# Kernel optimization log

Measured on AMD Instinct MI355X. Metric: run time of the kernel, lower is better.

## Reference

```python
import jax, jax.numpy as jnp
import numpy as np

D_MODEL = 1024
NUM_HEADS = 16
HEAD_DIM = D_MODEL // NUM_HEADS
SCALE = HEAD_DIM ** -0.5
LN_EPS = 1e-5
Q_EPS = 1e-5


def bit_quant(W):
    # BitNet b1.58 ternary weight quantization with straight-through estimator.
    gamma = jnp.mean(jnp.abs(W))
    Wq = jnp.clip(jnp.round(W / (gamma + Q_EPS)), -1.0, 1.0) * gamma
    return W + jax.lax.stop_gradient(Wq - W)


def layer_norm(x, gamma, beta):
    mu = jnp.mean(x, axis=-1, keepdims=True)
    var = jnp.mean(jnp.square(x - mu), axis=-1, keepdims=True)
    return (x - mu) * jax.lax.rsqrt(var + LN_EPS) * gamma + beta


def setup_inputs() -> dict:
    key = jax.random.key(0)
    ks = jax.random.split(key, 8)
    B, T, T_ctx, C = 4, 1024, 2048, D_MODEL
    w_std = C ** -0.5
    return {
        "x": jax.random.normal(ks[0], (B, T, C), jnp.float32),
        "context": jax.random.normal(ks[1], (B, T_ctx, C), jnp.float32),
        "Wq": jax.random.normal(ks[2], (C, C), jnp.float32) * w_std,
        "bq": jnp.zeros((C,), jnp.float32),
        "Wk": jax.random.normal(ks[3], (C, C), jnp.float32) * w_std,
        "bk": jnp.zeros((C,), jnp.float32),
        "Wv": jax.random.normal(ks[4], (C, C), jnp.float32) * w_std,
        "bv": jnp.zeros((C,), jnp.float32),
        "Wo": jax.random.normal(ks[5], (C, C), jnp.float32) * w_std,
        "bo": jnp.zeros((C,), jnp.float32),
        "ln_gamma": jnp.ones((C,), jnp.float32),
        "ln_beta": jnp.zeros((C,), jnp.float32),
    }


def reference(x, context, Wq, bq, Wk, bk, Wv, bv, Wo, bo, ln_gamma, ln_beta):
    B, T, C = x.shape
    T_ctx = context.shape[1]
    residual = x
    xn = layer_norm(x, ln_gamma, ln_beta)
    # BitNet-quantized projections (torch Linear: y = x @ W.T + b)
    q = xn @ bit_quant(Wq).T + bq                      # [B,T,C]
    k = context @ bit_quant(Wk).T + bk                 # [B,T_ctx,C]
    v = context @ bit_quant(Wv).T + bv                 # [B,T_ctx,C]
    q = q.reshape(B, T, NUM_HEADS, HEAD_DIM)
    k = k.reshape(B, T_ctx, NUM_HEADS, HEAD_DIM)
    v = v.reshape(B, T_ctx, NUM_HEADS, HEAD_DIM)
    scores = jnp.einsum("bqhd,bkhd->bhqk", q, k) * SCALE   # [B,H,T,T_ctx]
    probs = jax.nn.softmax(scores, axis=-1)
    out = jnp.einsum("bhqk,bkhd->bqhd", probs, v).reshape(B, T, C)
    return residual + (out @ bit_quant(Wo).T + bo)
```

## Files before the change

### kernel.cpp

```cpp
#include <hip/hip_runtime.h>
#include <hip/hip_bf16.h>

typedef __attribute__((ext_vector_type(8))) short s8x;
typedef __attribute__((ext_vector_type(4))) float f4x;
typedef unsigned short u16;
typedef unsigned int u32;

#define T_ 1024
#define TC_ 2048
#define SCLOG2E 0.1803368801111243f

#define WAIT_VM(n) asm volatile("s_waitcnt vmcnt(" #n ")" ::: "memory")

__device__ __forceinline__ u16 f2bf(float f) {
    u32 u = __float_as_uint(f);
    return (u16)((u + 0x7fffu + ((u >> 16) & 1u)) >> 16);
}

#if defined(__has_builtin)
#if __has_builtin(__builtin_amdgcn_cvt_pk_bf16_f32)
#define HAVE_PK 1
#endif
#endif

__device__ __forceinline__ u32 pack2bf(float a, float b) {
#ifdef HAVE_PK
    typedef __attribute__((ext_vector_type(2))) __bf16 bf2t;
    bf2t r = __builtin_amdgcn_cvt_pk_bf16_f32(a, b);
    u32 u;
    __builtin_memcpy(&u, &r, 4);
    return u;
#else
    return (u32)f2bf(a) | ((u32)f2bf(b) << 16);
#endif
}

__device__ __forceinline__ void gload16(const void* g, void* l) {
    __builtin_amdgcn_global_load_lds((const __attribute__((address_space(1))) u32*)g,
                                     (__attribute__((address_space(3))) u32*)l, 16, 0, 0);
}

__global__ __launch_bounds__(256) void absmean_k(const float* __restrict__ W0, const float* __restrict__ W1,
                                                 const float* __restrict__ W2, const float* __restrict__ W3,
                                                 float* __restrict__ gsum) {
    int wi = blockIdx.y;
    const float* W = (wi == 0) ? W0 : (wi == 1) ? W1 : (wi == 2) ? W2 : W3;
    const int n4 = (1024 * 1024) / 4;
    float s = 0.f;
    int stride = gridDim.x * blockDim.x;
    for (int i = blockIdx.x * blockDim.x + threadIdx.x; i < n4; i += stride) {
        float4 v = ((const float4*)W)[i];
        s += fabsf(v.x) + fabsf(v.y) + fabsf(v.z) + fabsf(v.w);
    }
#pragma unroll
    for (int off = 32; off; off >>= 1) s += __shfl_down(s, off, 64);
    __shared__ float ps[4];
    if ((threadIdx.x & 63) == 0) ps[threadIdx.x >> 6] = s;
    __syncthreads();
    if (threadIdx.x == 0) atomicAdd(gsum + wi, ps[0] + ps[1] + ps[2] + ps[3]);
}

__global__ __launch_bounds__(256) void prep_k(
        const float* __restrict__ x, const float* __restrict__ lng, const float* __restrict__ lnb,
        u16* __restrict__ xn,
        const float* __restrict__ ctx, u16* __restrict__ ctxb,
        const float* __restrict__ W0, const float* __restrict__ W1,
        const float* __restrict__ W2, const float* __restrict__ W3,
        u16* __restrict__ D0, u16* __restrict__ D1, u16* __restrict__ D2, u16* __restrict__ D3,
        const float* __restrict__ gsum) {
    __shared__ float ps[8];
    int bx = blockIdx.x, t = threadIdx.x;
    if (bx < 4096) {
        int row = bx;
        float4 xv = ((const float4*)(x + (long)row * 1024))[t];
        float s = xv.x + xv.y + xv.z + xv.w;
        float s2 = xv.x * xv.x + xv.y * xv.y + xv.z * xv.z + xv.w * xv.w;
#pragma unroll
        for (int off = 32; off; off >>= 1) { s += __shfl_down(s, off, 64); s2 += __shfl_down(s2, off, 64); }
        if ((t & 63) == 0) { ps[t >> 6] = s; ps[4 + (t >> 6)] = s2; }
        __syncthreads();
        float S = ps[0] + ps[1] + ps[2] + ps[3];
        float S2 = ps[4] + ps[5] + ps[6] + ps[7];
        float mu = S * (1.f / 1024.f);
        float var = S2 * (1.f / 1024.f) - mu * mu;
        float rstd = rsqrtf(var + 1e-5f);
        float4 gv = ((const float4*)lng)[t];
        float4 bv = ((const float4*)lnb)[t];
        uint2 o;
        o.x = pack2bf((xv.x - mu) * rstd * gv.x + bv.x, (xv.y - mu) * rstd * gv.y + bv.y);
        o.y = pack2bf((xv.z - mu) * rstd * gv.z + bv.z, (xv.w - mu) * rstd * gv.w + bv.w);
        ((uint2*)(xn + (long)row * 1024))[t] = o;
    } else if (bx < 12288) {
        int i = (bx - 4096) * 256 + t;
        float4 v = ((const float4*)ctx)[i];
        uint2 o = {pack2bf(v.x, v.y), pack2bf(v.z, v.w)};
        ((uint2*)ctxb)[i] = o;
    } else {
        int wi = (bx - 12288) >> 10;
        const float* W = (wi == 0) ? W0 : (wi == 1) ? W1 : (wi == 2) ? W2 : W3;
        u16* D = (wi == 0) ? D0 : (wi == 1) ? D1 : (wi == 2) ? D2 : D3;
        float inv = 1.0f / (gsum[wi] * (1.0f / 1048576.0f) + 1e-5f);
        int i = ((bx - 12288) & 1023) * 256 + t;
        float4 wv = ((const float4*)W)[i];
        uint2 o;
        o.x = pack2bf(fminf(1.f, fmaxf(-1.f, rintf(wv.x * inv))),
                      fminf(1.f, fmaxf(-1.f, rintf(wv.y * inv))));
        o.y = pack2bf(fminf(1.f, fmaxf(-1.f, rintf(wv.z * inv))),
                      fminf(1.f, fmaxf(-1.f, rintf(wv.w * inv))));
        ((uint2*)D)[i] = o;
    }
}

__global__ __launch_bounds__(256) void gemm_fused(
        const u16* __restrict__ xn, const u16* __restrict__ ctxb,
        const u16* __restrict__ wtq, const u16* __restrict__ wtk, const u16* __restrict__ wtv,
        const float* __restrict__ bq, const float* __restrict__ bk, const float* __restrict__ bv,
        const float* __restrict__ gsum,
        u16* __restrict__ qb, u16* __restrict__ kb, u16* __restrict__ vtb) {
    __shared__ __align__(16) char smem[49152];
    int tid = threadIdx.x;
    int w = tid >> 6, l = tid & 63, lq = l & 15, lh = l >> 4;
    int wm = (w >> 1) * 64, wn = (w & 1) * 64;
    int bx = blockIdx.x;
    int xcd = bx & 7;
    int prob, m0, n0, gidx;
    const u16 *A, *Wt;
    const float* bias;
    float sc;
    if (bx < 256) {
        int local = bx >> 3;
        prob = 0; A = xn; Wt = wtq; bias = bq; sc = SCLOG2E; gidx = 0;
        m0 = (xcd * 4 + (local & 3)) * 128;
        n0 = (local >> 2) * 128;
    } else {
        int b = bx - 256;
        int local3 = b >> 3;
        int kv = local3 & 1;
        int idx = local3 >> 1;
        prob = 1 + kv; A = ctxb;
        Wt = kv ? wtv : wtk; bias = kv ? bv : bk; sc = 1.0f; gidx = 1 + kv;
        m0 = (xcd * 8 + (idx & 7)) * 128;
        n0 = (idx >> 3) * 128;
    }
    int sp = tid >> 3, ss = tid & 7;
    int st = ss ^ (sp & 7);
    int r0 = sp * 2 + (st >> 2), c0 = st & 3;
    const u16* Ag0 = A + (long)(m0 + r0) * 1024 + c0 * 8;
    const u16* Ag1 = Ag0 + 64 * 1024;
    const u16* Bg0 = Wt + (long)(n0 + r0) * 1024 + c0 * 8;
    const u16* Bg1 = Bg0 + 64 * 1024;
    int aoff[4], boff[4];
#pragma unroll
    for (int i = 0; i < 4; i++) {
        int ar = wm + i * 16 + lq, ap = ar >> 1;
        aoff[i] = ap * 128 + (((((ar & 1) << 2) | lh) ^ (ap & 7)) * 16);
        int br = wn + i * 16 + lq, bp = br >> 1;
        boff[i] = bp * 128 + (((((br & 1) << 2) | lh) ^ (bp & 7)) * 16);
    }
    f4x acc[4][4] = {};
#define STAGE_G(kt, buf)                                                   \
    {                                                                      \
        char* Ad = smem + (buf) * 16384;                                   \
        char* Bd = Ad + 8192;                                              \
        gload16(Ag0 + (kt) * 32, Ad + tid * 16);                           \
        gload16(Ag1 + (kt) * 32, Ad + 4096 + tid * 16);                    \
        gload16(Bg0 + (kt) * 32, Bd + tid * 16);                           \
        gload16(Bg1 + (kt) * 32, Bd + 4096 + tid * 16);                    \
    }
    STAGE_G(0, 0);
    STAGE_G(1, 1);
#pragma unroll
    for (int kt = 0; kt < 32; kt++) {
        if (kt < 31) { WAIT_VM(4); } else { WAIT_VM(0); }
        __builtin_amdgcn_s_barrier();
        if (kt + 2 < 32) STAGE_G(kt + 2, (kt + 2) % 3);
        const char* Ac = smem + (kt % 3) * 16384;
        const char* Bc = Ac + 8192;
        s8x af[4], bfr[4];
#pragma unroll
        for (int i = 0; i < 4; i++) {
            af[i] = *(const s8x*)(Ac + aoff[i]);
            bfr[i] = *(const s8x*)(Bc + boff[i]);
        }
#pragma unroll
        for (int i = 0; i < 4; i++)
#pragma unroll
            for (int j = 0; j < 4; j++)
                acc[i][j] = __builtin_amdgcn_mfma_f32_16x16x32_bf16(af[i], bfr[j], acc[i][j], 0, 0, 0);
    }
    float gamma = gsum[gidx] * (1.0f / 1048576.0f) * sc;
    if (prob < 2) {
        u16* outq = (prob == 0) ? qb : kb;
        int tshift = (prob == 0) ? 10 : 11;
        int tmask = (1 << tshift) - 1;
#pragma unroll
        for (int i = 0; i < 4; i++) {
            int gr = m0 + wm + i * 16 + lh * 4;
#pragma unroll
            for (int j = 0; j < 4; j++) {
                int gc = n0 + wn + j * 16 + lq;
                float bb = bias[gc] * sc;
                int h = gc >> 6, d = gc & 63;
#pragma unroll
                for (int r = 0; r < 4; r++) {
                    int row = gr + r;
                    int bidx = row >> tshift, tt = row & tmask;
                    outq[((((long)(bidx * 16 + h)) << tshift) + tt) * 64 + d] = f2bf(acc[i][j][r] * gamma + bb);
                }
            }
        }
    } else {
        __syncthreads();
        char* Ct = smem;
#pragma unroll
        for (int i = 0; i < 4; i++) {
            int tt = wm + i * 16 + lh * 4;
#pragma unroll
            for (int j = 0; j < 4; j++) {
                int c = wn + j * 16 + lq;
                float bb = bias[n0 + c];
                uint2 pk;
                pk.x = pack2bf(acc[i][j][0] * gamma + bb, acc[i][j][1] * gamma + bb);
                pk.y = pack2bf(acc[i][j][2] * gamma + bb, acc[i][j][3] * gamma + bb);
                int slot = (tt >> 3) ^ (c & 15);
                *(uint2*)(Ct + c * 256 + slot * 16 + (tt & 7) * 2) = pk;
            }
        }
        __syncthreads();
        int bb2 = m0 >> 11, t0 = m0 & 2047;
#pragma unroll
        for (int it = 0; it < 8; it++) {
            int e = it * 256 + tid;
            int c = e >> 4, ch = e & 15;
            int slot = ch ^ (c & 15);
            s8x v = *(const s8x*)(Ct + c * 256 + slot * 16);
            int gcg = n0 + c;
            int h = gcg >> 6, d = gcg & 63;
            *(s8x*)(vtb + ((long)((bb2 * 16 + h) * 64 + d)) * TC_ + t0 + ch * 8) = v;
        }
    }
}

__global__ __launch_bounds__(256) void gemm_o(const u16* __restrict__ A, const u16* __restrict__ Wt,
                                              const float* __restrict__ bias, const float* __restrict__ gsum,
                                              const float* __restrict__ residual, float* __restrict__ outr) {
    __shared__ __align__(16) char smem[36864];
    int tid = threadIdx.x;
    int w = tid >> 6, l = tid & 63, lq = l & 15, lh = l >> 4;
    int wm = (w >> 1) * 64, wn = (w & 1) * 32;
    int bx = blockIdx.x;
    int xcd = bx & 7, local = bx >> 3;
    int m0 = (xcd * 4 + (local & 3)) * 128;
    int n0 = (local >> 2) * 64;
    int sp = tid >> 3, ss = tid & 7;
    int st = ss ^ (sp & 7);
    int r0 = sp * 2 + (st >> 2), c0 = st & 3;
    const u16* Ag0 = A + (long)(m0 + r0) * 1024 + c0 * 8;
    const u16* Ag1 = Ag0 + 64 * 1024;
    const u16* Bg0 = Wt + (long)(n0 + r0) * 1024 + c0 * 8;
    int aoff[4], boff[2];
#pragma unroll
    for (int i = 0; i < 4; i++) {
        int ar = wm + i * 16 + lq, ap = ar >> 1;
        aoff[i] = ap * 128 + (((((ar & 1) << 2) | lh) ^ (ap & 7)) * 16);
    }
#pragma unroll
    for (int j = 0; j < 2; j++) {
        int br = wn + j * 16 + lq, bp = br >> 1;
        boff[j] = bp * 128 + (((((br & 1) << 2) | lh) ^ (bp & 7)) * 16);
    }
    f4x acc[4][2] = {};
#define STAGE_O(kt, buf)                                                   \
    {                                                                      \
        char* Ad = smem + (buf) * 12288;                                   \
        char* Bd = Ad + 8192;                                              \
        gload16(Ag0 + (kt) * 32, Ad + tid * 16);                           \
        gload16(Ag1 + (kt) * 32, Ad + 4096 + tid * 16);                    \
        gload16(Bg0 + (kt) * 32, Bd + tid * 16);                           \
    }
    STAGE_O(0, 0);
    STAGE_O(1, 1);
#pragma unroll
    for (int kt = 0; kt < 32; kt++) {
        if (kt < 31) { WAIT_VM(3); } else { WAIT_VM(0); }
        __builtin_amdgcn_s_barrier();
        if (kt + 2 < 32) STAGE_O(kt + 2, (kt + 2) % 3);
        const char* Ac = smem + (kt % 3) * 12288;
        const char* Bc = Ac + 8192;
        s8x af[4], bfr[2];
#pragma unroll
        for (int i = 0; i < 4; i++) af[i] = *(const s8x*)(Ac + aoff[i]);
#pragma unroll
        for (int j = 0; j < 2; j++) bfr[j] = *(const s8x*)(Bc + boff[j]);
#pragma unroll
        for (int i = 0; i < 4; i++)
#pragma unroll
            for (int j = 0; j < 2; j++)
                acc[i][j] = __builtin_amdgcn_mfma_f32_16x16x32_bf16(af[i], bfr[j], acc[i][j], 0, 0, 0);
    }
    float gamma = gsum[3] * (1.0f / 1048576.0f);
#pragma unroll
    for (int i = 0; i < 4; i++) {
        int gr = m0 + wm + i * 16 + lh * 4;
#pragma unroll
        for (int j = 0; j < 2; j++) {
            int gc = n0 + wn + j * 16 + lq;
            float bb = bias[gc];
#pragma unroll
            for (int r = 0; r < 4; r++) {
                long idx = (long)(gr + r) * 1024 + gc;
                outr[idx] = residual[idx] + acc[i][j][r] * gamma + bb;
            }
        }
    }
}

__global__ __launch_bounds__(256) void attn_k(const u16* __restrict__ qh, const u16* __restrict__ kh,
                                              const u16* __restrict__ vth, u16* __restrict__ attn) {
    __shared__ __align__(16) char smem[51200];
    int tid = threadIdx.x, w = tid >> 6, l = tid & 63, lq = l & 15, lh = l >> 4;
    int bh = blockIdx.x, q0 = blockIdx.y * 128;
    const u16* qp = qh + ((long)bh * T_ + q0) * 64;
    const u16* kp = kh + (long)bh * TC_ * 64;
    const u16* vp = vth + (long)bh * 64 * TC_;
#pragma unroll
    for (int i = 0; i < 4; i++) {
        int cid = i * 256 + tid;
        int r = cid >> 3, c = (cid & 7) ^ (r & 7);
        gload16(qp + r * 64 + c * 8, smem + cid * 16);
    }
    __syncthreads();
    s8x qf[2][2];
#pragma unroll
    for (int nb = 0; nb < 2; nb++)
#pragma unroll
        for (int dh = 0; dh < 2; dh++) {
            int qrow = w * 32 + nb * 16 + lq;
            int ch = (dh * 4 + lh) ^ (qrow & 7);
            qf[nb][dh] = *(const s8x*)(smem + qrow * 128 + ch * 16);
        }
    __syncthreads();
#define STAGE_KV(kt, buf)                                                          \
    {                                                                              \
        char* Kb = smem + (buf) * 16384;                                           \
        char* Vb = Kb + 8192;                                                      \
        _Pragma("unroll") for (int i = 0; i < 2; i++) {                            \
            int cid = i * 256 + tid;                                               \
            int r = cid >> 3, c = (cid & 7) ^ (r & 7);                             \
            gload16(kp + ((kt) * 64 + r) * 64 + c * 8, Kb + cid * 16);             \
            gload16(vp + (long)r * TC_ + (kt) * 64 + c * 8, Vb + cid * 16);        \
        }                                                                          \
    }
    STAGE_KV(0, 0);
    f4x oacc[2][4] = {};
    f4x lrun[2] = {};
    const s8x ones = {16256, 16256, 16256, 16256, 16256, 16256, 16256, 16256};
    char* Psb = smem + 32768 + w * 4608;
    for (int kt = 0; kt < TC_ / 64; kt++) {
        __syncthreads();
        if (kt + 1 < TC_ / 64) STAGE_KV(kt + 1, (kt + 1) & 1);
        char* Ksb = smem + (kt & 1) * 16384;
        char* Vsb = Ksb + 8192;
        f4x z[2][4];
#pragma unroll
        for (int ni = 0; ni < 4; ni++) {
            int kr = ni * 16 + lq;
            s8x a0 = *(const s8x*)(Ksb + kr * 128 + ((lh) ^ (kr & 7)) * 16);
            s8x a1 = *(const s8x*)(Ksb + kr * 128 + ((4 + lh) ^ (kr & 7)) * 16);
#pragma unroll
            for (int nb = 0; nb < 2; nb++) {
                f4x zz = {0.f, 0.f, 0.f, 0.f};
                zz = __builtin_amdgcn_mfma_f32_16x16x32_bf16(a0, qf[nb][0], zz, 0, 0, 0);
                zz = __builtin_amdgcn_mfma_f32_16x16x32_bf16(a1, qf[nb][1], zz, 0, 0, 0);
                z[nb][ni] = zz;
            }
        }
#pragma unroll
        for (int nb = 0; nb < 2; nb++) {
            int prow = nb * 16 + lq;
#pragma unroll
            for (int ni = 0; ni < 4; ni++) {
                uint2 pk;
                pk.x = pack2bf(__builtin_amdgcn_exp2f(z[nb][ni][0]), __builtin_amdgcn_exp2f(z[nb][ni][1]));
                pk.y = pack2bf(__builtin_amdgcn_exp2f(z[nb][ni][2]), __builtin_amdgcn_exp2f(z[nb][ni][3]));
                *(uint2*)(Psb + prow * 144 + ni * 32 + lh * 8) = pk;
            }
        }
        s8x vf[4][2];
#pragma unroll
        for (int nd = 0; nd < 4; nd++) {
            int vr = nd * 16 + lq;
            vf[nd][0] = *(const s8x*)(Vsb + vr * 128 + ((lh) ^ (vr & 7)) * 16);
            vf[nd][1] = *(const s8x*)(Vsb + vr * 128 + ((4 + lh) ^ (vr & 7)) * 16);
        }
#pragma unroll
        for (int qb = 0; qb < 2; qb++) {
            int prow = qb * 16 + lq;
            s8x pf0 = *(const s8x*)(Psb + prow * 144 + lh * 16);
            s8x pf1 = *(const s8x*)(Psb + prow * 144 + 64 + lh * 16);
            f4x rs = {0.f, 0.f, 0.f, 0.f};
            rs = __builtin_amdgcn_mfma_f32_16x16x32_bf16(pf0, ones, rs, 0, 0, 0);
            rs = __builtin_amdgcn_mfma_f32_16x16x32_bf16(pf1, ones, rs, 0, 0, 0);
#pragma unroll
            for (int r = 0; r < 4; r++) lrun[qb][r] += rs[r];
#pragma unroll
            for (int nd = 0; nd < 4; nd++) {
                oacc[qb][nd] = __builtin_amdgcn_mfma_f32_16x16x32_bf16(pf0, vf[nd][0], oacc[qb][nd], 0, 0, 0);
                oacc[qb][nd] = __builtin_amdgcn_mfma_f32_16x16x32_bf16(pf1, vf[nd][1], oacc[qb][nd], 0, 0, 0);
            }
        }
    }
    int b = bh >> 4, h = bh & 15;
#pragma unroll
    for (int qb = 0; qb < 2; qb++)
#pragma unroll
        for (int r = 0; r < 4; r++) {
            int q = q0 + w * 32 + qb * 16 + lh * 4 + r;
            float rcp = 1.f / lrun[qb][r];
#pragma unroll
            for (int nd = 0; nd < 4; nd++)
                attn[((long)(b * T_ + q)) * 1024 + h * 64 + nd * 16 + lq] = f2bf(oacc[qb][nd][r] * rcp);
        }
}

extern "C" void kernel_launch(void* const* d_in, const int* in_sizes, int n_in,
                              void* d_out, int out_size, void* d_ws, size_t ws_size,
                              hipStream_t stream) {
    const float* x   = (const float*)d_in[0];
    const float* ctx = (const float*)d_in[1];
    const float* Wq  = (const float*)d_in[2];
    const float* bq  = (const float*)d_in[3];
    const float* Wk  = (const float*)d_in[4];
    const float* bk  = (const float*)d_in[5];
    const float* Wv  = (const float*)d_in[6];
    const float* bv  = (const float*)d_in[7];
    const float* Wo  = (const float*)d_in[8];
    const float* bo  = (const float*)d_in[9];
    const float* lng = (const float*)d_in[10];
    const float* lnb = (const float*)d_in[11];
    float* out = (float*)d_out;

    char* ws = (char*)d_ws;
    float* gsum = (float*)ws;
    size_t off = 256;
    u16* wtq  = (u16*)(ws + off); off += (size_t)1024 * 1024 * 2;
    u16* wtk  = (u16*)(ws + off); off += (size_t)1024 * 1024 * 2;
    u16* wtv  = (u16*)(ws + off); off += (size_t)1024 * 1024 * 2;
    u16* wto  = (u16*)(ws + off); off += (size_t)1024 * 1024 * 2;
    u16* ctxb = (u16*)(ws + off); off += (size_t)8192 * 1024 * 2;
    u16* xn   = (u16*)(ws + off); off += (size_t)4096 * 1024 * 2;
    u16* qb_  = (u16*)(ws + off); off += (size_t)4096 * 1024 * 2;
    u16* kb   = (u16*)(ws + off); off += (size_t)8192 * 1024 * 2;
    u16* vtb  = (u16*)(ws + off); off += (size_t)8192 * 1024 * 2;
    u16* attnb = xn;

    hipMemsetAsync(gsum, 0, 16, stream);
    absmean_k<<<dim3(128, 4), 256, 0, stream>>>(Wq, Wk, Wv, Wo, gsum);
    prep_k<<<16384, 256, 0, stream>>>(x, lng, lnb, xn, ctx, ctxb,
                                      Wq, Wk, Wv, Wo, wtq, wtk, wtv, wto, gsum);
    gemm_fused<<<1280, 256, 0, stream>>>(xn, ctxb, wtq, wtk, wtv, bq, bk, bv, gsum, qb_, kb, vtb);
    attn_k<<<dim3(64, 8), 256, 0, stream>>>(qb_, kb, vtb, attnb);
    gemm_o<<<512, 256, 0, stream>>>(attnb, wto, bo, gsum, x, out);
}
```

Before: 254.2 us.

## Keep attention probabilities in registers via permlane swaps, halve query tile

The attention kernel no longer writes exp'd scores to LDS and reads them back as MFMA A-operands. It rearranges them in registers with permlane32/permlane16 swaps, and adds s_setprio around the MFMA sections. The query tile per block drops from 128 to 64 rows (16 per wave), doubling the grid, shrinking LDS to 32KB and raising occupancy. The cost is that each K/V tile is now loaded by twice as many blocks, so K/V global and LDS traffic is doubled per unit of compute.

```diff
diff --git a/kernel.cpp b/kernel.cpp
--- a/kernel.cpp
+++ b/kernel.cpp
@@ -20,6 +20,9 @@
 #if defined(__has_builtin)
 #if __has_builtin(__builtin_amdgcn_cvt_pk_bf16_f32)
 #define HAVE_PK 1
+#endif
+#if __has_builtin(__builtin_amdgcn_permlane16_swap) && __has_builtin(__builtin_amdgcn_permlane32_swap)
+#define HAVE_PLSWAP 1
 #endif
 #endif
 
@@ -32,6 +35,25 @@
     return u;
 #else
     return (u32)f2bf(a) | ((u32)f2bf(b) << 16);
+#endif
+}
+
+__device__ __forceinline__ void pswap32(u32& a, u32& b) {
+#ifdef HAVE_PLSWAP
+    typedef __attribute__((ext_vector_type(2))) unsigned int u2x;
+    u2x r = __builtin_amdgcn_permlane32_swap(a, b, false, false);
+    a = r.x; b = r.y;
+#else
+    asm("v_permlane32_swap_b32 %0, %1" : "+v"(a), "+v"(b));
+#endif
+}
+__device__ __forceinline__ void pswap16(u32& a, u32& b) {
+#ifdef HAVE_PLSWAP
+    typedef __attribute__((ext_vector_type(2))) unsigned int u2x;
+    u2x r = __builtin_amdgcn_permlane16_swap(a, b, false, false);
+    a = r.x; b = r.y;
+#else
+    asm("v_permlane16_swap_b32 %0, %1" : "+v"(a), "+v"(b));
 #endif
 }
 
@@ -317,28 +339,26 @@
 
 __global__ __launch_bounds__(256) void attn_k(const u16* __restrict__ qh, const u16* __restrict__ kh,
                                               const u16* __restrict__ vth, u16* __restrict__ attn) {
-    __shared__ __align__(16) char smem[51200];
+    __shared__ __align__(16) char smem[32768];
     int tid = threadIdx.x, w = tid >> 6, l = tid & 63, lq = l & 15, lh = l >> 4;
-    int bh = blockIdx.x, q0 = blockIdx.y * 128;
+    int bh = blockIdx.x, q0 = blockIdx.y * 64;
     const u16* qp = qh + ((long)bh * T_ + q0) * 64;
     const u16* kp = kh + (long)bh * TC_ * 64;
     const u16* vp = vth + (long)bh * 64 * TC_;
 #pragma unroll
-    for (int i = 0; i < 4; i++) {
+    for (int i = 0; i < 2; i++) {
         int cid = i * 256 + tid;
         int r = cid >> 3, c = (cid & 7) ^ (r & 7);
         gload16(qp + r * 64 + c * 8, smem + cid * 16);
     }
     __syncthreads();
-    s8x qf[2][2];
-#pragma unroll
-    for (int nb = 0; nb < 2; nb++)
-#pragma unroll
-        for (int dh = 0; dh < 2; dh++) {
-            int qrow = w * 32 + nb * 16 + lq;
-            int ch = (dh * 4 + lh) ^ (qrow & 7);
-            qf[nb][dh] = *(const s8x*)(smem + qrow * 128 + ch * 16);
-        }
+    s8x qf[2];
+#pragma unroll
+    for (int dh = 0; dh < 2; dh++) {
+        int qrow = w * 16 + lq;
+        int ch = (dh * 4 + lh) ^ (qrow & 7);
+        qf[dh] = *(const s8x*)(smem + qrow * 128 + ch * 16);
+    }
     __syncthreads();
 #define STAGE_KV(kt, buf)                                                          \
     {                                                                              \
@@ -352,40 +372,27 @@
         }                                                                          \
     }
     STAGE_KV(0, 0);
-    f4x oacc[2][4] = {};
-    f4x lrun[2] = {};
+    f4x oacc[4] = {};
+    f4x lrun = {};
     const s8x ones = {16256, 16256, 16256, 16256, 16256, 16256, 16256, 16256};
-    char* Psb = smem + 32768 + w * 4608;
     for (int kt = 0; kt < TC_ / 64; kt++) {
         __syncthreads();
         if (kt + 1 < TC_ / 64) STAGE_KV(kt + 1, (kt + 1) & 1);
         char* Ksb = smem + (kt & 1) * 16384;
         char* Vsb = Ksb + 8192;
-        f4x z[2][4];
+        f4x z[4];
+        __builtin_amdgcn_s_setprio(1);
 #pragma unroll
         for (int ni = 0; ni < 4; ni++) {
             int kr = ni * 16 + lq;
             s8x a0 = *(const s8x*)(Ksb + kr * 128 + ((lh) ^ (kr & 7)) * 16);
             s8x a1 = *(const s8x*)(Ksb + kr * 128 + ((4 + lh) ^ (kr & 7)) * 16);
-#pragma unroll
-            for (int nb = 0; nb < 2; nb++) {
-                f4x zz = {0.f, 0.f, 0.f, 0.f};
-                zz = __builtin_amdgcn_mfma_f32_16x16x32_bf16(a0, qf[nb][0], zz, 0, 0, 0);
-                zz = __builtin_amdgcn_mfma_f32_16x16x32_bf16(a1, qf[nb][1], zz, 0, 0, 0);
-                z[nb][ni] = zz;
-            }
-        }
-#pragma unroll
-        for (int nb = 0; nb < 2; nb++) {
-            int prow = nb * 16 + lq;
-#pragma unroll
-            for (int ni = 0; ni < 4; ni++) {
-                uint2 pk;
-                pk.x = pack2bf(__builtin_amdgcn_exp2f(z[nb][ni][0]), __builtin_amdgcn_exp2f(z[nb][ni][1]));
-                pk.y = pack2bf(__builtin_amdgcn_exp2f(z[nb][ni][2]), __builtin_amdgcn_exp2f(z[nb][ni][3]));
-                *(uint2*)(Psb + prow * 144 + ni * 32 + lh * 8) = pk;
-            }
-        }
+            f4x zz = {0.f, 0.f, 0.f, 0.f};
+            zz = __builtin_amdgcn_mfma_f32_16x16x32_bf16(a0, qf[0], zz, 0, 0, 0);
+            zz = __builtin_amdgcn_mfma_f32_16x16x32_bf16(a1, qf[1], zz, 0, 0, 0);
+            z[ni] = zz;
+        }
+        __builtin_amdgcn_s_setprio(0);
         s8x vf[4][2];
 #pragma unroll
         for (int nd = 0; nd < 4; nd++) {
@@ -393,34 +400,43 @@
             vf[nd][0] = *(const s8x*)(Vsb + vr * 128 + ((lh) ^ (vr & 7)) * 16);
             vf[nd][1] = *(const s8x*)(Vsb + vr * 128 + ((4 + lh) ^ (vr & 7)) * 16);
         }
-#pragma unroll
-        for (int qb = 0; qb < 2; qb++) {
-            int prow = qb * 16 + lq;
-            s8x pf0 = *(const s8x*)(Psb + prow * 144 + lh * 16);
-            s8x pf1 = *(const s8x*)(Psb + prow * 144 + 64 + lh * 16);
-            f4x rs = {0.f, 0.f, 0.f, 0.f};
-            rs = __builtin_amdgcn_mfma_f32_16x16x32_bf16(pf0, ones, rs, 0, 0, 0);
-            rs = __builtin_amdgcn_mfma_f32_16x16x32_bf16(pf1, ones, rs, 0, 0, 0);
-#pragma unroll
-            for (int r = 0; r < 4; r++) lrun[qb][r] += rs[r];
-#pragma unroll
-            for (int nd = 0; nd < 4; nd++) {
-                oacc[qb][nd] = __builtin_amdgcn_mfma_f32_16x16x32_bf16(pf0, vf[nd][0], oacc[qb][nd], 0, 0, 0);
-                oacc[qb][nd] = __builtin_amdgcn_mfma_f32_16x16x32_bf16(pf1, vf[nd][1], oacc[qb][nd], 0, 0, 0);
-            }
-        }
+        u32 Wp[4][2];
+#pragma unroll
+        for (int ni = 0; ni < 4; ni++) {
+            Wp[ni][0] = pack2bf(__builtin_amdgcn_exp2f(z[ni][0]), __builtin_amdgcn_exp2f(z[ni][1]));
+            Wp[ni][1] = pack2bf(__builtin_amdgcn_exp2f(z[ni][2]), __builtin_amdgcn_exp2f(z[ni][3]));
+        }
+        u32 a0w = Wp[0][0], a1w = Wp[1][0]; pswap32(a0w, a1w); pswap16(a0w, a1w);
+        u32 b0w = Wp[0][1], b1w = Wp[1][1]; pswap32(b0w, b1w); pswap16(b0w, b1w);
+        u32 c0w = Wp[2][0], c1w = Wp[3][0]; pswap32(c0w, c1w); pswap16(c0w, c1w);
+        u32 d0w = Wp[2][1], d1w = Wp[3][1]; pswap32(d0w, d1w); pswap16(d0w, d1w);
+        u32 pw0[4] = {a0w, b0w, a1w, b1w};
+        u32 pw1[4] = {c0w, d0w, c1w, d1w};
+        s8x pf0, pf1;
+        __builtin_memcpy(&pf0, pw0, 16);
+        __builtin_memcpy(&pf1, pw1, 16);
+        __builtin_amdgcn_s_setprio(1);
+        f4x rs = {0.f, 0.f, 0.f, 0.f};
+        rs = __builtin_amdgcn_mfma_f32_16x16x32_bf16(pf0, ones, rs, 0, 0, 0);
+        rs = __builtin_amdgcn_mfma_f32_16x16x32_bf16(pf1, ones, rs, 0, 0, 0);
+#pragma unroll
+        for (int r = 0; r < 4; r++) lrun[r] += rs[r];
+#pragma unroll
+        for (int nd = 0; nd < 4; nd++) {
+            oacc[nd] = __builtin_amdgcn_mfma_f32_16x16x32_bf16(pf0, vf[nd][0], oacc[nd], 0, 0, 0);
+            oacc[nd] = __builtin_amdgcn_mfma_f32_16x16x32_bf16(pf1, vf[nd][1], oacc[nd], 0, 0, 0);
+        }
+        __builtin_amdgcn_s_setprio(0);
     }
     int b = bh >> 4, h = bh & 15;
 #pragma unroll
-    for (int qb = 0; qb < 2; qb++)
-#pragma unroll
-        for (int r = 0; r < 4; r++) {
-            int q = q0 + w * 32 + qb * 16 + lh * 4 + r;
-            float rcp = 1.f / lrun[qb][r];
-#pragma unroll
-            for (int nd = 0; nd < 4; nd++)
-                attn[((long)(b * T_ + q)) * 1024 + h * 64 + nd * 16 + lq] = f2bf(oacc[qb][nd][r] * rcp);
-        }
+    for (int r = 0; r < 4; r++) {
+        int q = q0 + w * 16 + lh * 4 + r;
+        float rcp = 1.f / lrun[r];
+#pragma unroll
+        for (int nd = 0; nd < 4; nd++)
+            attn[((long)(b * T_ + q)) * 1024 + h * 64 + nd * 16 + lq] = f2bf(oacc[nd][r] * rcp);
+    }
 }
 
 extern "C" void kernel_launch(void* const* d_in, const int* in_sizes, int n_in,
@@ -459,6 +475,6 @@
     prep_k<<<16384, 256, 0, stream>>>(x, lng, lnb, xn, ctx, ctxb,
                                       Wq, Wk, Wv, Wo, wtq, wtk, wtv, wto, gsum);
     gemm_fused<<<1280, 256, 0, stream>>>(xn, ctxb, wtq, wtk, wtv, bq, bk, bv, gsum, qb_, kb, vtb);
-    attn_k<<<dim3(64, 8), 256, 0, stream>>>(qb_, kb, vtb, attnb);
+    attn_k<<<dim3(64, 16), 256, 0, stream>>>(qb_, kb, vtb, attnb);
     gemm_o<<<512, 256, 0, stream>>>(attnb, wto, bo, gsum, x, out);
 }
```

Result: no change. 251.8 us (-1.0%).
